# Optimization experiments

Hardware: AMD Instinct MI355X
Metric: run time of the kernel (lower is better)

## Reference

```python
import jax, jax.numpy as jnp
import numpy as np

B, S, D = 4, 4096, 128

def setup_inputs() -> dict:
    key = jax.random.key(0)
    kq, kk, kv = jax.random.split(key, 3)
    q = jax.random.normal(kq, (B, S, D), dtype=jnp.float32)
    k = jax.random.normal(kk, (B, S, D), dtype=jnp.float32)
    v = jax.random.normal(kv, (B, S, D), dtype=jnp.float32)
    return {"q": q, "k": k, "v": v}

def reference(q, k, v):
    d_model = q.shape[-1]
    scale = 1.0 / jnp.sqrt(jnp.asarray(d_model, q.dtype))
    # [B, S, S] scores
    scores = jnp.einsum('bqd,bkd->bqk', q, k) * scale
    s = q.shape[1]
    causal = jnp.tril(jnp.ones((s, s), dtype=bool))
    neg_inf = jnp.asarray(-jnp.inf, scores.dtype)
    scores = jnp.where(causal[None, :, :], scores, neg_inf)
    attn = jax.nn.softmax(scores, axis=-1)
    return jnp.einsum('bqk,bkd->bqd', attn, v)
```

## Files before the change

### kernel.cpp

```cpp
#include <hip/hip_runtime.h>


#define B_   4
#define S_   4096
#define D_   128
#define BN   64
#define NT_  64
#define QT_  32
#define RMAX 4
#define BLOB_SHORTS 16384
#define MASKVAL (-1.0e30f)

typedef __attribute__((ext_vector_type(8))) short bf16x8;
typedef __attribute__((ext_vector_type(4))) float f32x4;

__device__ __forceinline__ short f2bf(float x) {
    unsigned u = __builtin_bit_cast(unsigned, x);
    unsigned r = (u + 0x7fffu + ((u >> 16) & 1u)) >> 16;
    return (short)r;
}
__device__ __forceinline__ float ex2(float x) { return __builtin_amdgcn_exp2f(x); }
__device__ __forceinline__ unsigned pkbf(float lo, float hi) {
    return (unsigned)(unsigned short)f2bf(lo) | ((unsigned)(unsigned short)f2bf(hi) << 16);
}
__device__ __forceinline__ void gl_lds16(const short* g, short* l) {
    __builtin_amdgcn_global_load_lds(
        (const __attribute__((address_space(1))) unsigned int*)g,
        (__attribute__((address_space(3))) unsigned int*)l, 16, 0, 0);
}

__global__ __launch_bounds__(256) void prep(const float* __restrict__ Qg,
                                            const float* __restrict__ Kg,
                                            const float* __restrict__ Vg,
                                            short* __restrict__ Qbf,
                                            short* __restrict__ KV)
{
    __shared__ short vt[64][40];
    const int id  = blockIdx.x;
    const int tid = threadIdx.x;
    const float SC = 0.12751740f;

    if (id < 1024) {
        const int b = id & 3, tile = (id >> 2) & 63, q4 = id >> 8;
        const int n = q4 * 16 + (tid >> 4);
        const int G = tid & 15;
        const size_t rowoff = ((size_t)b * S_ + (size_t)tile * 64 + n) * D_ + G * 8;
        short* blob = KV + (size_t)(b * NT_ + tile) * BLOB_SHORTS;
        {
            float4 a = *reinterpret_cast<const float4*>(Qg + rowoff);
            float4 c = *reinterpret_cast<const float4*>(Qg + rowoff + 4);
            bf16x8 v;
            v[0] = f2bf(a.x * SC); v[1] = f2bf(a.y * SC); v[2] = f2bf(a.z * SC); v[3] = f2bf(a.w * SC);
            v[4] = f2bf(c.x * SC); v[5] = f2bf(c.y * SC); v[6] = f2bf(c.z * SC); v[7] = f2bf(c.w * SC);
            *reinterpret_cast<bf16x8*>(Qbf + rowoff) = v;
        }
        {
            float4 a = *reinterpret_cast<const float4*>(Kg + rowoff);
            float4 c = *reinterpret_cast<const float4*>(Kg + rowoff + 4);
            bf16x8 v;
            v[0] = f2bf(a.x); v[1] = f2bf(a.y); v[2] = f2bf(a.z); v[3] = f2bf(a.w);
            v[4] = f2bf(c.x); v[5] = f2bf(c.y); v[6] = f2bf(c.z); v[7] = f2bf(c.w);
            const int p = (G & 8) | ((G & 7) ^ (n & 7));
            *reinterpret_cast<bf16x8*>(blob + n * 128 + p * 8) = v;
        }
    } else {
        const int u = id - 1024;
        const int b = u & 3, tile = (u >> 2) & 63, dq = u >> 8;
        short* blob = KV + (size_t)(b * NT_ + tile) * BLOB_SHORTS;
        {
            const int n = tid >> 2, c8 = tid & 3;
            const size_t off = ((size_t)b * S_ + (size_t)tile * 64 + n) * D_ + dq * 32 + c8 * 8;
            float4 a = *reinterpret_cast<const float4*>(Vg + off);
            float4 c = *reinterpret_cast<const float4*>(Vg + off + 4);
            bf16x8 v;
            v[0] = f2bf(a.x); v[1] = f2bf(a.y); v[2] = f2bf(a.z); v[3] = f2bf(a.w);
            v[4] = f2bf(c.x); v[5] = f2bf(c.y); v[6] = f2bf(c.z); v[7] = f2bf(c.w);
            *reinterpret_cast<bf16x8*>(&vt[n][c8 * 8]) = v;
        }
        __syncthreads();
        {
            const int dl = tid >> 3, G = tid & 7;
            const int d  = dq * 32 + dl;
            bf16x8 g;
#pragma unroll
            for (int i = 0; i < 8; ++i) g[i] = vt[G * 8 + i][dl];
            const int p = G ^ (d & 7);
            *reinterpret_cast<bf16x8*>(blob + 8192 + d * 64 + p * 8) = g;
        }
    }
}

template<bool SPLIT>
__global__ __launch_bounds__(512, 4) void fa_fwd(const short* __restrict__ Qbf,
                                                 const short* __restrict__ KV,
                                                 float* __restrict__ Og,
                                                 float* __restrict__ Op,
                                                 float* __restrict__ Ml,
                                                 int R)
{
    __shared__ short lkv[2][BLOB_SHORTS];

    const int tid  = threadIdx.x;
    const int wv   = tid >> 6;
    const int lane = tid & 63;
    const int m    = lane & 15;
    const int quad = lane >> 4;
    const int m7   = m & 7;

    int batch, t, lo, hi, chunk_id;
    {
        const int id = blockIdx.x;
        batch = id & 3;
        if (SPLIT) {
            int u = id >> 2;
            int tt = u / R;
            int r  = u - tt * R;
            t  = QT_ - 1 - tt;
            const int nk = 2 * t + 2;
            lo = r * nk / R;
            hi = (r + 1) * nk / R;
            chunk_id = (batch * QT_ + t) * R + r;
            if (lo >= hi) return;
        } else {
            t  = QT_ - 1 - (id >> 2);
            lo = 0; hi = 2 * t + 2; chunk_id = 0;
        }
    }

    bf16x8 qf[4];
    {
        const short* qp = Qbf + ((size_t)batch * S_ + (size_t)t * 128 + wv * 16 + m) * D_ + quad * 8;
#pragma unroll
        for (int c = 0; c < 4; ++c)
            qf[c] = *reinterpret_cast<const bf16x8*>(qp + c * 32);
    }

    f32x4 acc[8];
#pragma unroll
    for (int i = 0; i < 8; ++i) acc[i] = (f32x4){0.f, 0.f, 0.f, 0.f};
    float mrun = MASKVAL, lrun = 0.f;

    const size_t tilebase = (size_t)batch * NT_ * BLOB_SHORTS;
#define STAGE(KT, BUF) do {                                                   \
        const short* g_ = KV + tilebase + (size_t)(KT) * BLOB_SHORTS + tid * 8;\
        short* l_ = (BUF) + tid * 8;                                          \
        _Pragma("unroll")                                                     \
        for (int c_ = 0; c_ < 4; ++c_)                                        \
            gl_lds16(g_ + c_ * 4096, l_ + c_ * 4096);                         \
    } while (0)

    STAGE(lo, lkv[0]);

    for (int kt = lo; kt < hi; ++kt) {
        const short* cur = lkv[(kt - lo) & 1];
        short* nxt = lkv[(kt - lo + 1) & 1];
        __syncthreads();
        if (kt + 1 < hi) STAGE(kt + 1, nxt);

        const short* lk = cur;
        const short* lv = cur + 8192;

        f32x4 st[4];
#pragma unroll
        for (int nt = 0; nt < 4; ++nt) st[nt] = (f32x4){0.f, 0.f, 0.f, 0.f};
#pragma unroll
        for (int c = 0; c < 4; ++c) {
            const int p = ((c >> 1) * 8) | ((((c & 1) * 4) | quad) ^ m7);
#pragma unroll
            for (int nt = 0; nt < 4; ++nt) {
                bf16x8 kf = *reinterpret_cast<const bf16x8*>(lk + nt * 2048 + m * 128 + p * 8);
                st[nt] = __builtin_amdgcn_mfma_f32_16x16x32_bf16(kf, qf[c], st[nt], 0, 0, 0);
            }
        }

        if (kt >= 2 * t) {
            const int kbase = (kt - 2 * t) * 64;
            const int qloc  = wv * 16 + m;
#pragma unroll
            for (int nt = 0; nt < 4; ++nt)
#pragma unroll
                for (int r = 0; r < 4; ++r)
                    if (kbase + nt * 16 + quad * 4 + r > qloc) st[nt][r] = MASKVAL;
        }

        float mx = MASKVAL;
#pragma unroll
        for (int nt = 0; nt < 4; ++nt)
#pragma unroll
            for (int r = 0; r < 4; ++r) mx = fmaxf(mx, st[nt][r]);
        mx = fmaxf(mx, __shfl_xor(mx, 16));
        mx = fmaxf(mx, __shfl_xor(mx, 32));
        const float mnew = fmaxf(mrun, mx);
        const float al   = ex2(mrun - mnew);
        mrun = mnew;
        float sum = 0.f;
#pragma unroll
        for (int nt = 0; nt < 4; ++nt)
#pragma unroll
            for (int r = 0; r < 4; ++r) {
                float pv = ex2(st[nt][r] - mnew);
                st[nt][r] = pv;
                sum += pv;
            }
        sum += __shfl_xor(sum, 16);
        sum += __shfl_xor(sum, 32);
        lrun = lrun * al + sum;
#pragma unroll
        for (int r = 0; r < 4; ++r) {
            float alq = __shfl(al, quad * 4 + r);
#pragma unroll
            for (int ct = 0; ct < 8; ++ct) acc[ct][r] *= alq;
        }

        const int srcA = ((quad & 1) << 5) + m;
        const int srcB = srcA + 16;
        const bool loq = quad < 2;
#pragma unroll
        for (int ks = 0; ks < 2; ++ks) {
            unsigned pk0 = pkbf(st[2 * ks][0],     st[2 * ks][1]);
            unsigned pk1 = pkbf(st[2 * ks][2],     st[2 * ks][3]);
            unsigned pk2 = pkbf(st[2 * ks + 1][0], st[2 * ks + 1][1]);
            unsigned pk3 = pkbf(st[2 * ks + 1][2], st[2 * ks + 1][3]);
            unsigned w0a = __shfl((int)pk0, srcA);
            unsigned w0b = __shfl((int)pk2, srcA);
            unsigned w1a = __shfl((int)pk1, srcA);
            unsigned w1b = __shfl((int)pk3, srcA);
            unsigned w2a = __shfl((int)pk0, srcB);
            unsigned w2b = __shfl((int)pk2, srcB);
            unsigned w3a = __shfl((int)pk1, srcB);
            unsigned w3b = __shfl((int)pk3, srcB);
            int4 wi;
            wi.x = (int)(loq ? w0a : w0b);
            wi.y = (int)(loq ? w1a : w1b);
            wi.z = (int)(loq ? w2a : w2b);
            wi.w = (int)(loq ? w3a : w3b);
            bf16x8 pf = __builtin_bit_cast(bf16x8, wi);
            const int p = (ks * 4 + quad) ^ m7;
#pragma unroll
            for (int ct = 0; ct < 8; ++ct) {
                bf16x8 vf = *reinterpret_cast<const bf16x8*>(lv + ct * 1024 + m * 64 + p * 8);
                acc[ct] = __builtin_amdgcn_mfma_f32_16x16x32_bf16(pf, vf, acc[ct], 0, 0, 0);
            }
        }
    }
#undef STAGE

    const int row0 = wv * 16 + quad * 4;
    if (SPLIT) {
        float* ob = Op + (size_t)chunk_id * (128 * D_);
#pragma unroll
        for (int r = 0; r < 4; ++r)
#pragma unroll
            for (int ct = 0; ct < 8; ++ct)
                ob[(row0 + r) * D_ + ct * 16 + m] = acc[ct][r];
        if (lane < 16) {
            float* mlb = Ml + (size_t)chunk_id * (128 * 2) + (wv * 16 + lane) * 2;
            mlb[0] = mrun;
            mlb[1] = lrun;
        }
    } else {
        const float inv = 1.0f / lrun;
        const size_t obase = ((size_t)batch * S_ + (size_t)t * 128 + row0) * D_;
#pragma unroll
        for (int r = 0; r < 4; ++r) {
            float invq = __shfl(inv, quad * 4 + r);
#pragma unroll
            for (int ct = 0; ct < 8; ++ct)
                Og[obase + (size_t)r * D_ + ct * 16 + m] = acc[ct][r] * invq;
        }
    }
}

template<int RR>
__global__ __launch_bounds__(256) void fa_merge(const float* __restrict__ Op,
                                                const float* __restrict__ Ml,
                                                float* __restrict__ Og)
{
    const int x   = blockIdx.x;
    const int btq = x >> 4;
    const int oct = x & 15;
    const int t   = btq & (QT_ - 1);
    const int nk  = 2 * t + 2;
    const int row = oct * 8 + (threadIdx.x >> 5);
    const int cg  = threadIdx.x & 31;
    const size_t cbase = (size_t)btq * RR;

    float mg = MASKVAL;
#pragma unroll
    for (int r = 0; r < RR; ++r) {
        int lo = r * nk / RR, hi = (r + 1) * nk / RR;
        if (lo < hi) mg = fmaxf(mg, Ml[(cbase + r) * (128 * 2) + row * 2]);
    }
    float l = 0.f;
    f32x4 a = (f32x4){0.f, 0.f, 0.f, 0.f};
#pragma unroll
    for (int r = 0; r < RR; ++r) {
        int lo = r * nk / RR, hi = (r + 1) * nk / RR;
        if (lo >= hi) continue;
        float mr = Ml[(cbase + r) * (128 * 2) + row * 2];
        float lr = Ml[(cbase + r) * (128 * 2) + row * 2 + 1];
        float w  = ex2(mr - mg);
        l += lr * w;
        a += w * *reinterpret_cast<const f32x4*>(Op + (cbase + r) * (128 * D_) + row * D_ + cg * 4);
    }
    *reinterpret_cast<f32x4*>(Og + (size_t)btq * (128 * D_) + row * D_ + cg * 4) = a * (1.0f / l);
}

extern "C" void kernel_launch(void* const* d_in, const int* in_sizes, int n_in,
                              void* d_out, int out_size, void* d_ws, size_t ws_size,
                              hipStream_t stream) {
    const float* q = (const float*)d_in[0];
    const float* k = (const float*)d_in[1];
    const float* v = (const float*)d_in[2];
    float* o = (float*)d_out;

    const size_t QBF_BYTES = (size_t)B_ * S_ * D_ * 2;
    const size_t KV_BYTES  = (size_t)B_ * NT_ * BLOB_SHORTS * 2;
    const size_t PREFIX    = QBF_BYTES + KV_BYTES;
    const size_t O_FLOATS  = (size_t)B_ * QT_ * 128 * D_;
    const size_t ML_FLOATS = (size_t)B_ * QT_ * 128 * 2;
    const size_t PER_R     = (O_FLOATS + ML_FLOATS) * sizeof(float);

    char* ws = (char*)d_ws;
    short* Qbf = (short*)ws;
    short* KV  = (short*)(ws + QBF_BYTES);

    int R = 0;
    if (ws_size > PREFIX) {
        R = (int)((ws_size - PREFIX) / PER_R);
        if (R > RMAX) R = RMAX;
    }

    prep<<<dim3(2048), 256, 0, stream>>>(q, k, v, Qbf, KV);

    if (R >= 1) {
        float* Op = (float*)(ws + PREFIX);
        float* Ml = Op + (size_t)R * O_FLOATS;
        fa_fwd<true><<<dim3(B_ * QT_ * R), 512, 0, stream>>>(Qbf, KV, nullptr, Op, Ml, R);
        switch (R) {
            case 1: fa_merge<1><<<dim3(B_ * QT_ * 16), 256, 0, stream>>>(Op, Ml, o); break;
            case 2: fa_merge<2><<<dim3(B_ * QT_ * 16), 256, 0, stream>>>(Op, Ml, o); break;
            case 3: fa_merge<3><<<dim3(B_ * QT_ * 16), 256, 0, stream>>>(Op, Ml, o); break;
            default: fa_merge<4><<<dim3(B_ * QT_ * 16), 256, 0, stream>>>(Op, Ml, o); break;
        }
    } else {
        fa_fwd<false><<<dim3(B_ * QT_), 512, 0, stream>>>(Qbf, KV, o, nullptr, nullptr, 1);
    }
}
```

Measured before the change: 123.4 us.

## Balance split-KV chunks per q-tile, defer softmax rescale, skip masked waves, add setprio

Replaces the uniform R-way split with a variable chunk count per q-tile, about ten K tiles per chunk, so causal work is spread more evenly across blocks. The running-max rescale of the accumulators is now skipped unless the max grows by more than a threshold. The row-sum shuffle reduction moves out of the loop to the end. Waves whose rows lie entirely above a K tile skip compute, and s_setprio is raised around the MFMA sections. The costs are more partial outputs to write and merge, a larger workspace requirement that falls back to the unsplit path if not met, and reliance on a threshold so that deferred exponentials do not overflow.

```diff
diff --git a/kernel.cpp b/kernel.cpp
--- a/kernel.cpp
+++ b/kernel.cpp
@@ -7,12 +7,17 @@
 #define BN   64
 #define NT_  64
 #define QT_  32
-#define RMAX 4
+#define NCHB 119
 #define BLOB_SHORTS 16384
 #define MASKVAL (-1.0e30f)
+#define DEFER_THR 8.0f
 
 typedef __attribute__((ext_vector_type(8))) short bf16x8;
 typedef __attribute__((ext_vector_type(4))) float f32x4;
+
+__device__ __host__ __forceinline__ constexpr int chunks_of(int t) { return (2 * t + 11) / 10; }
+constexpr int nchb_calc() { int s = 0; for (int t = 0; t < QT_; ++t) s += chunks_of(t); return s; }
+static_assert(nchb_calc() == NCHB, "chunk count mismatch");
 
 __device__ __forceinline__ short f2bf(float x) {
     unsigned u = __builtin_bit_cast(unsigned, x);
@@ -95,8 +100,7 @@
                                                  const short* __restrict__ KV,
                                                  float* __restrict__ Og,
                                                  float* __restrict__ Op,
-                                                 float* __restrict__ Ml,
-                                                 int R)
+                                                 float* __restrict__ Ml)
 {
     __shared__ short lkv[2][BLOB_SHORTS];
 
@@ -111,20 +115,21 @@
     {
         const int id = blockIdx.x;
         batch = id & 3;
+        int u = id >> 2;
         if (SPLIT) {
-            int u = id >> 2;
-            int tt = u / R;
-            int r  = u - tt * R;
-            t  = QT_ - 1 - tt;
+            int tt = QT_ - 1, base = 0, rt;
+            for (;;) { rt = chunks_of(tt); if (u < base + rt) break; base += rt; --tt; }
+            t = tt;
+            const int r  = u - base;
             const int nk = 2 * t + 2;
-            lo = r * nk / R;
-            hi = (r + 1) * nk / R;
-            chunk_id = (batch * QT_ + t) * R + r;
-            if (lo >= hi) return;
+            lo = r * nk / rt;
+            hi = (r + 1) * nk / rt;
+            chunk_id = batch * NCHB + u;
         } else {
-            t  = QT_ - 1 - (id >> 2);
+            t  = QT_ - 1 - u;
             lo = 0; hi = 2 * t + 2; chunk_id = 0;
         }
+        if (lo >= hi) return;
     }
 
     bf16x8 qf[4];
@@ -141,6 +146,7 @@
     float mrun = MASKVAL, lrun = 0.f;
 
     const size_t tilebase = (size_t)batch * NT_ * BLOB_SHORTS;
+    const int qtop = t * 128 + wv * 16 + 15;
 #define STAGE(KT, BUF) do {                                                   \
         const short* g_ = KV + tilebase + (size_t)(KT) * BLOB_SHORTS + tid * 8;\
         short* l_ = (BUF) + tid * 8;                                          \
@@ -157,12 +163,15 @@
         __syncthreads();
         if (kt + 1 < hi) STAGE(kt + 1, nxt);
 
+        if (kt * 64 > qtop) continue;
+
         const short* lk = cur;
         const short* lv = cur + 8192;
 
         f32x4 st[4];
 #pragma unroll
         for (int nt = 0; nt < 4; ++nt) st[nt] = (f32x4){0.f, 0.f, 0.f, 0.f};
+        __builtin_amdgcn_s_setprio(1);
 #pragma unroll
         for (int c = 0; c < 4; ++c) {
             const int p = ((c >> 1) * 8) | ((((c & 1) * 4) | quad) ^ m7);
@@ -172,6 +181,7 @@
                 st[nt] = __builtin_amdgcn_mfma_f32_16x16x32_bf16(kf, qf[c], st[nt], 0, 0, 0);
             }
         }
+        __builtin_amdgcn_s_setprio(0);
 
         if (kt >= 2 * t) {
             const int kbase = (kt - 2 * t) * 64;
@@ -190,27 +200,28 @@
             for (int r = 0; r < 4; ++r) mx = fmaxf(mx, st[nt][r]);
         mx = fmaxf(mx, __shfl_xor(mx, 16));
         mx = fmaxf(mx, __shfl_xor(mx, 32));
-        const float mnew = fmaxf(mrun, mx);
-        const float al   = ex2(mrun - mnew);
-        mrun = mnew;
+        if (__any(mx - mrun > DEFER_THR)) {
+            const float mnew = fmaxf(mrun, mx);
+            const float al   = ex2(mrun - mnew);
+            mrun = mnew;
+            lrun *= al;
+#pragma unroll
+            for (int r = 0; r < 4; ++r) {
+                float alq = __shfl(al, quad * 4 + r);
+#pragma unroll
+                for (int ct = 0; ct < 8; ++ct) acc[ct][r] *= alq;
+            }
+        }
         float sum = 0.f;
 #pragma unroll
         for (int nt = 0; nt < 4; ++nt)
 #pragma unroll
             for (int r = 0; r < 4; ++r) {
-                float pv = ex2(st[nt][r] - mnew);
+                float pv = ex2(st[nt][r] - mrun);
                 st[nt][r] = pv;
                 sum += pv;
             }
-        sum += __shfl_xor(sum, 16);
-        sum += __shfl_xor(sum, 32);
-        lrun = lrun * al + sum;
-#pragma unroll
-        for (int r = 0; r < 4; ++r) {
-            float alq = __shfl(al, quad * 4 + r);
-#pragma unroll
-            for (int ct = 0; ct < 8; ++ct) acc[ct][r] *= alq;
-        }
+        lrun += sum;
 
         const int srcA = ((quad & 1) << 5) + m;
         const int srcB = srcA + 16;
@@ -236,14 +247,19 @@
             wi.w = (int)(loq ? w3a : w3b);
             bf16x8 pf = __builtin_bit_cast(bf16x8, wi);
             const int p = (ks * 4 + quad) ^ m7;
+            __builtin_amdgcn_s_setprio(1);
 #pragma unroll
             for (int ct = 0; ct < 8; ++ct) {
                 bf16x8 vf = *reinterpret_cast<const bf16x8*>(lv + ct * 1024 + m * 64 + p * 8);
                 acc[ct] = __builtin_amdgcn_mfma_f32_16x16x32_bf16(pf, vf, acc[ct], 0, 0, 0);
             }
+            __builtin_amdgcn_s_setprio(0);
         }
     }
 #undef STAGE
+
+    lrun += __shfl_xor(lrun, 16);
+    lrun += __shfl_xor(lrun, 32);
 
     const int row0 = wv * 16 + quad * 4;
     if (SPLIT) {
@@ -271,7 +287,6 @@
     }
 }
 
-template<int RR>
 __global__ __launch_bounds__(256) void fa_merge(const float* __restrict__ Op,
                                                 const float* __restrict__ Ml,
                                                 float* __restrict__ Og)
@@ -280,29 +295,35 @@
     const int btq = x >> 4;
     const int oct = x & 15;
     const int t   = btq & (QT_ - 1);
-    const int nk  = 2 * t + 2;
+    const int b   = btq >> 5;
+    const int rt  = chunks_of(t);
+    int base = 0;
+    for (int tt = QT_ - 1; tt > t; --tt) base += chunks_of(tt);
+    const int cbase = b * NCHB + base;
     const int row = oct * 8 + (threadIdx.x >> 5);
     const int cg  = threadIdx.x & 31;
-    const size_t cbase = (size_t)btq * RR;
-
+
+    float mr_[7], lr_[7];
     float mg = MASKVAL;
 #pragma unroll
-    for (int r = 0; r < RR; ++r) {
-        int lo = r * nk / RR, hi = (r + 1) * nk / RR;
-        if (lo < hi) mg = fmaxf(mg, Ml[(cbase + r) * (128 * 2) + row * 2]);
-    }
+    for (int r = 0; r < 7; ++r)
+        if (r < rt) {
+            float2 ml2 = *reinterpret_cast<const float2*>(
+                Ml + (size_t)(cbase + r) * (128 * 2) + row * 2);
+            mr_[r] = ml2.x;
+            lr_[r] = ml2.y;
+            mg = fmaxf(mg, mr_[r]);
+        }
     float l = 0.f;
     f32x4 a = (f32x4){0.f, 0.f, 0.f, 0.f};
 #pragma unroll
-    for (int r = 0; r < RR; ++r) {
-        int lo = r * nk / RR, hi = (r + 1) * nk / RR;
-        if (lo >= hi) continue;
-        float mr = Ml[(cbase + r) * (128 * 2) + row * 2];
-        float lr = Ml[(cbase + r) * (128 * 2) + row * 2 + 1];
-        float w  = ex2(mr - mg);
-        l += lr * w;
-        a += w * *reinterpret_cast<const f32x4*>(Op + (cbase + r) * (128 * D_) + row * D_ + cg * 4);
-    }
+    for (int r = 0; r < 7; ++r)
+        if (r < rt) {
+            float w = ex2(mr_[r] - mg);
+            l += lr_[r] * w;
+            a += w * *reinterpret_cast<const f32x4*>(
+                Op + (size_t)(cbase + r) * (128 * D_) + row * D_ + cg * 4);
+        }
     *reinterpret_cast<f32x4*>(Og + (size_t)btq * (128 * D_) + row * D_ + cg * 4) = a * (1.0f / l);
 }
 
@@ -317,33 +338,23 @@
     const size_t QBF_BYTES = (size_t)B_ * S_ * D_ * 2;
     const size_t KV_BYTES  = (size_t)B_ * NT_ * BLOB_SHORTS * 2;
     const size_t PREFIX    = QBF_BYTES + KV_BYTES;
-    const size_t O_FLOATS  = (size_t)B_ * QT_ * 128 * D_;
-    const size_t ML_FLOATS = (size_t)B_ * QT_ * 128 * 2;
-    const size_t PER_R     = (O_FLOATS + ML_FLOATS) * sizeof(float);
+    const int    NCH       = B_ * NCHB;
+    const size_t O_FLOATS  = (size_t)NCH * 128 * D_;
+    const size_t ML_FLOATS = (size_t)NCH * 128 * 2;
+    const size_t NEEDED    = PREFIX + (O_FLOATS + ML_FLOATS) * sizeof(float);
 
     char* ws = (char*)d_ws;
     short* Qbf = (short*)ws;
     short* KV  = (short*)(ws + QBF_BYTES);
 
-    int R = 0;
-    if (ws_size > PREFIX) {
-        R = (int)((ws_size - PREFIX) / PER_R);
-        if (R > RMAX) R = RMAX;
-    }
-
     prep<<<dim3(2048), 256, 0, stream>>>(q, k, v, Qbf, KV);
 
-    if (R >= 1) {
+    if (ws_size >= NEEDED) {
         float* Op = (float*)(ws + PREFIX);
-        float* Ml = Op + (size_t)R * O_FLOATS;
-        fa_fwd<true><<<dim3(B_ * QT_ * R), 512, 0, stream>>>(Qbf, KV, nullptr, Op, Ml, R);
-        switch (R) {
-            case 1: fa_merge<1><<<dim3(B_ * QT_ * 16), 256, 0, stream>>>(Op, Ml, o); break;
-            case 2: fa_merge<2><<<dim3(B_ * QT_ * 16), 256, 0, stream>>>(Op, Ml, o); break;
-            case 3: fa_merge<3><<<dim3(B_ * QT_ * 16), 256, 0, stream>>>(Op, Ml, o); break;
-            default: fa_merge<4><<<dim3(B_ * QT_ * 16), 256, 0, stream>>>(Op, Ml, o); break;
-        }
+        float* Ml = Op + O_FLOATS;
+        fa_fwd<true><<<dim3(NCH), 512, 0, stream>>>(Qbf, KV, nullptr, Op, Ml);
+        fa_merge<<<dim3(B_ * QT_ * 16), 256, 0, stream>>>(Op, Ml, o);
     } else {
-        fa_fwd<false><<<dim3(B_ * QT_), 512, 0, stream>>>(Qbf, KV, o, nullptr, nullptr, 1);
-    }
-}
+        fa_fwd<false><<<dim3(B_ * QT_), 512, 0, stream>>>(Qbf, KV, o, nullptr, nullptr);
+    }
+}
```

Measured after the change: 117.4 us. -4.9%, faster.
